# Optimization experiments

Hardware: AMD Instinct MI355X
Metric: run time of the kernel (lower is better)

## Reference

```python
import jax, jax.numpy as jnp
import numpy as np

N = 30000   # fluid particles
E = 480000  # edges
F = 4       # fluidFeatures (in channels)
P = 8       # RBF basis size per dim (dims=[8], 1D)
LAYERS = [32, 64, 64, 2]


def hat_basis(x, n):
    # 'linear' RBF: hat functions on n evenly spaced centers in [-1, 1]
    centers = jnp.linspace(-1.0, 1.0, n, dtype=x.dtype)
    spacing = 2.0 / (n - 1)
    return jnp.maximum(0.0, 1.0 - jnp.abs(x[:, None] - centers[None, :]) / spacing)  # [E, n]


def rbf_conv(x, fi, fj, d, W, b, mask, n_nodes):
    # x: [N, Cin]; d: [E, 1] clamped; W: [P, Cin, Cout]; b: [Cout]
    phi = hat_basis(d[:, 0], W.shape[0])      # [E, P]
    xj = x[fj]                                 # gather source features [E, Cin]
    msg = jnp.zeros((xj.shape[0], W.shape[2]), dtype=x.dtype)
    for p in range(W.shape[0]):                # small fixed P=8 loop keeps memory O(E*Cout)
        msg = msg + phi[:, p, None] * (xj @ W[p])
    msg = jnp.where(mask[:, None], msg, 0.0)   # centerIgnore: drop self edges fi==fj
    out = jax.ops.segment_sum(msg, fi, num_segments=n_nodes)  # scatter-reduce to targets
    return out + b


def _xavier(key, shape_in, shape_out):
    lim = float(np.sqrt(6.0 / (shape_in + shape_out)))
    return jax.random.uniform(key, (shape_in, shape_out), jnp.float32, -lim, lim)


def setup_inputs() -> dict:
    key = jax.random.key(0)
    ks = jax.random.split(key, 16)
    fluidFeatures = jax.random.normal(ks[0], (N, F), jnp.float32)
    fi = jax.random.randint(ks[1], (E,), 0, N)
    fj = jax.random.randint(ks[2], (E,), 0, N)
    distances = jax.random.normal(ks[3], (E, 1), jnp.float32)
    # conv channels: 4->32, 64->64, 64->64, 64->2
    cio = [(F, 32), (2 * 32, 64), (64, 64), (64, 2)]
    inp = {"fluidFeatures": fluidFeatures, "fi": fi, "fj": fj, "distances": distances}
    for li, (ci, co) in enumerate(cio):
        inp[f"cW{li}"] = jax.random.normal(ks[4 + li], (P, ci, co), jnp.float32) * (1.0 / np.sqrt(P * ci))
        inp[f"cb{li}"] = jnp.zeros((co,), jnp.float32)
        inp[f"fW{li}"] = _xavier(ks[8 + li], ci, co)   # stored [in, out]
        inp[f"fb{li}"] = jnp.zeros((co,), jnp.float32)
    return inp


def reference(fluidFeatures, fi, fj, distances,
              cW0, cb0, fW0, fb0, cW1, cb1, fW1, fb1,
              cW2, cb2, fW2, fb2, cW3, cb3, fW3, fb3):
    n_nodes = fluidFeatures.shape[0]
    mask = fi != fj                     # centerIgnore (mask instead of filter: jit-safe)
    d = jnp.clip(distances, -1.0, 1.0)

    conv0 = rbf_conv(fluidFeatures, fi, fj, d, cW0, cb0, mask, n_nodes)  # [N, 32]
    lin0 = fluidFeatures @ fW0 + fb0                                      # [N, 32]
    ans = jnp.concatenate([lin0, conv0], axis=1)                          # [N, 64]

    # i = 1: features[0]=32 != features[1]=64 -> no residual
    ansc = jax.nn.relu(ans)
    ans = rbf_conv(ansc, fi, fj, d, cW1, cb1, mask, n_nodes) + (ansc @ fW1 + fb1)
    # i = 2: features[1]==features[2]==64 and shapes match -> residual
    ansc = jax.nn.relu(ans)
    ans = rbf_conv(ansc, fi, fj, d, cW2, cb2, mask, n_nodes) + (ansc @ fW2 + fb2) + ans
    # i = 3: 64 -> 2, no residual
    ansc = jax.nn.relu(ans)
    ans = rbf_conv(ansc, fi, fj, d, cW3, cb3, mask, n_nodes) + (ansc @ fW3 + fb3)

    return ans  # dim == 1 (dims=[8]) -> no /128
```

## Files before the change

kernel.cpp:

```cpp
#include <hip/hip_runtime.h>


#define CAP 48

typedef __attribute__((ext_vector_type(8))) short short8;
typedef __attribute__((ext_vector_type(4))) float f32x4;
typedef int v4i __attribute__((ext_vector_type(4)));

__device__ __forceinline__ short bf16s(float f) {
  unsigned u = __float_as_uint(f);
  return (short)((u + 0x7FFF + ((u >> 16) & 1)) >> 16);
}
__device__ __forceinline__ float b2f(unsigned short s) {
  return __uint_as_float(((unsigned)s) << 16);
}
__device__ __forceinline__ unsigned pack2(float a, float b) {
  return (unsigned)(unsigned short)bf16s(a) | ((unsigned)(unsigned short)bf16s(b) << 16);
}
__device__ __forceinline__ float dec_w0(int v) {
  return __uint_as_float(0x3F800000u | (((unsigned)v & 0xFFFu) << 11)) - 1.0f;
}
__device__ __forceinline__ float dec_sf(int v) {
  return (float)(((unsigned)v >> 12) & 1u);
}
__device__ __forceinline__ unsigned long long rfl64(unsigned long long x) {
  unsigned lo = __builtin_amdgcn_readfirstlane((unsigned)x);
  unsigned hi = __builtin_amdgcn_readfirstlane((unsigned)(x >> 32));
  return ((unsigned long long)hi << 32) | (unsigned long long)lo;
}

#define LOAD_RECS32Q(JROW, CPTR, MRAW)                                      \
  v4i q0, q1, q2, q3, q4, q5, q6, q7;                                       \
  int MRAW;                                                                 \
  asm volatile("s_load_dwordx4 %0, %9, 0x0\n\t"                             \
               "s_load_dwordx4 %1, %9, 0x10\n\t"                            \
               "s_load_dwordx4 %2, %9, 0x20\n\t"                            \
               "s_load_dwordx4 %3, %9, 0x30\n\t"                            \
               "s_load_dwordx4 %4, %9, 0x40\n\t"                            \
               "s_load_dwordx4 %5, %9, 0x50\n\t"                            \
               "s_load_dwordx4 %6, %9, 0x60\n\t"                            \
               "s_load_dwordx4 %7, %9, 0x70\n\t"                            \
               "s_load_dword %8, %10, 0x0\n\t"                              \
               "s_waitcnt lgkmcnt(0)"                                       \
               : "=&s"(q0), "=&s"(q1), "=&s"(q2), "=&s"(q3), "=&s"(q4),     \
                 "=&s"(q5), "=&s"(q6), "=&s"(q7), "=&s"(MRAW)               \
               : "s"(JROW), "s"(CPTR)                                       \
               : "memory")

#define LOAD_RECS16TQ(JROW)                                                 \
  v4i qt0, qt1, qt2, qt3;                                                   \
  asm volatile("s_load_dwordx4 %0, %4, 0x80\n\t"                            \
               "s_load_dwordx4 %1, %4, 0x90\n\t"                            \
               "s_load_dwordx4 %2, %4, 0xA0\n\t"                            \
               "s_load_dwordx4 %3, %4, 0xB0\n\t"                            \
               "s_waitcnt lgkmcnt(0)"                                       \
               : "=&s"(qt0), "=&s"(qt1), "=&s"(qt2), "=&s"(qt3)             \
               : "s"(JROW)                                                  \
               : "memory")

#define RECK(K) ((K) < 4 ? q0[(K) & 3] : (K) < 8 ? q1[(K) & 3] :            \
                 (K) < 12 ? q2[(K) & 3] : (K) < 16 ? q3[(K) & 3] :          \
                 (K) < 20 ? q4[(K) & 3] : (K) < 24 ? q5[(K) & 3] :          \
                 (K) < 28 ? q6[(K) & 3] : q7[(K) & 3])
#define RECT(K) ((K) < 4 ? qt0[(K) & 3] : (K) < 8 ? qt1[(K) & 3] :          \
                 (K) < 12 ? qt2[(K) & 3] : qt3[(K) & 3])

__global__ void fill_prep(const float* __restrict__ dist,
                          const int* __restrict__ fi, const int* __restrict__ fj,
                          int* __restrict__ cnt, int* __restrict__ jw, int nE,
                          const float* __restrict__ cW0, const float* __restrict__ fW0,
                          const float* __restrict__ cW1, const float* __restrict__ fW1,
                          const float* __restrict__ cW2, const float* __restrict__ fW2,
                          const float* __restrict__ cW3,
                          short* __restrict__ W0T, short* __restrict__ W1T,
                          short* __restrict__ W2T, short* __restrict__ WT3,
                          const float* __restrict__ X,
                          unsigned short* __restrict__ Xb, int n,
                          int fillBlocks, int prepBlocks) {
  if ((int)blockIdx.x < fillBlocks) {
    int e = blockIdx.x * blockDim.x + threadIdx.x;
    if (e >= nE) return;
    int i = fi[e], j = fj[e];
    if (i == j) return;
    float d = fminf(1.0f, fmaxf(-1.0f, dist[e]));
    float u = (d + 1.0f) * 3.5f;
    int p = min((int)u, 6);
    float w0 = 1.0f - (u - (float)p);
    int wq = min((int)(w0 * 4096.0f + 0.5f), 4095);
    int pos = atomicAdd(&cnt[i], 1);
    if (pos < CAP)
      jw[(size_t)i * CAP + pos] =
          (int)(((unsigned)j << 17) | ((unsigned)p << 14) | 0x1000u | (unsigned)wq);
  } else if ((int)blockIdx.x < fillBlocks + prepBlocks) {
    int idx = ((int)blockIdx.x - fillBlocks) * blockDim.x + threadIdx.x;
    if (idx < 36864) {
      int o = idx / 576, k = idx - o * 576;
      float v = (k < 512) ? cW1[((size_t)(k >> 6) * 64 + (k & 63)) * 64 + o]
                          : fW1[(size_t)(k - 512) * 64 + o];
      W1T[idx] = bf16s(v);
    } else if (idx < 73728) {
      int r = idx - 36864;
      int o = r / 576, k = r - o * 576;
      float v = (k < 512) ? cW2[((size_t)(k >> 6) * 64 + (k & 63)) * 64 + o]
                          : fW2[(size_t)(k - 512) * 64 + o];
      W2T[r] = bf16s(v);
    } else if (idx < 77824) {
      int r = idx - 73728;
      int o = r >> 6, k = r & 63;
      float v = 0.0f;
      if (o < 32) {
        if (k >= 60) v = fW0[(size_t)(k - 60) * 32 + o];
      } else {
        if ((k & 7) < 4 && k < 60)
          v = cW0[((size_t)(k >> 3) * 4 + (k & 7)) * 32 + (o - 32)];
      }
      W0T[r] = bf16s(v);
    } else if (idx < 78848) {
      int r = idx - 77824;
      int t = r >> 6, ch = r & 63;
      WT3[r] = bf16s(cW3[((size_t)(t >> 1) * 64 + ch) * 2 + (t & 1)]);
    }
  } else {
    int idx = ((int)blockIdx.x - fillBlocks - prepBlocks) * blockDim.x + threadIdx.x;
    if (idx >= n * 8) return;
    int i = idx >> 3, c = idx & 7;
    float v = (c < 4) ? X[(size_t)i * 4 + c] : 0.0f;
    Xb[idx] = (unsigned short)bf16s(v);
  }
}

__global__ __launch_bounds__(1024, 8) void layer0_gemm(
    const unsigned short* __restrict__ Xb,
    const int* __restrict__ cnt, const int* __restrict__ jw,
    const float* __restrict__ cb0, const float* __restrict__ fb0,
    const short* __restrict__ W0T,
    unsigned short* __restrict__ ansc0, int n) {
  __shared__ __align__(16) unsigned short sA0[16 * 72];
  const int tid = threadIdx.x;
  const int w = tid >> 6;
  const int lane = tid & 63;
  const int s_lane = lane >> 3;
  const int k_lane = lane & 7;
  const int nodeBase = blockIdx.x * 16;
  const int i = nodeBase + w;
  const bool valid = (i < n);
  const int ic = valid ? i : 0;
  const int* jrow = (const int*)rfl64((unsigned long long)(jw + (size_t)ic * CAP));
  const int* cptr = (const int*)rfl64((unsigned long long)(cnt + ic));
  LOAD_RECS32Q(jrow, cptr, mraw);
  const int m = valid ? min(mraw, CAP) : 0;
  float acc = 0.0f;
#define L0E(K, RE)                                                          \
  { int v_ = RE(K);                                                         \
    const unsigned short* rp_ = Xb + ((size_t)((unsigned)v_ >> 17) << 3);   \
    float xv_ = b2f(rp_[k_lane]);                                           \
    float w0_ = dec_w0(v_);                                                 \
    float w1_ = dec_sf(v_) - w0_;                                           \
    int p_ = (int)(((unsigned)v_ >> 14) & 7u);                              \
    float sel_ = (s_lane == p_) ? w0_ : ((s_lane == p_ + 1) ? w1_ : 0.0f);  \
    acc = fmaf(sel_, xv_, acc); }
  L0E(0, RECK) L0E(1, RECK) L0E(2, RECK) L0E(3, RECK)
  L0E(4, RECK) L0E(5, RECK) L0E(6, RECK) L0E(7, RECK)
  L0E(8, RECK) L0E(9, RECK) L0E(10, RECK) L0E(11, RECK)
  L0E(12, RECK) L0E(13, RECK) L0E(14, RECK) L0E(15, RECK)
  if (m > 16) {
    L0E(16, RECK) L0E(17, RECK) L0E(18, RECK) L0E(19, RECK)
    L0E(20, RECK) L0E(21, RECK) L0E(22, RECK) L0E(23, RECK)
    L0E(24, RECK) L0E(25, RECK) L0E(26, RECK) L0E(27, RECK)
    L0E(28, RECK) L0E(29, RECK) L0E(30, RECK) L0E(31, RECK)
    if (m > 32) {
      LOAD_RECS16TQ(jrow);
      L0E(0, RECT) L0E(1, RECT) L0E(2, RECT) L0E(3, RECT)
      L0E(4, RECT) L0E(5, RECT) L0E(6, RECT) L0E(7, RECT)
      L0E(8, RECT) L0E(9, RECT) L0E(10, RECT) L0E(11, RECT)
      L0E(12, RECT) L0E(13, RECT) L0E(14, RECT) L0E(15, RECT)
    }
  }
#undef L0E
  float aout = acc;
  if (lane >= 60) aout = b2f(Xb[(size_t)ic * 8 + (lane - 60)]);
  sA0[w * 72 + lane] = (unsigned short)bf16s(aout);
  __syncthreads();
  if (w < 4) {
    const int mrow = lane & 15, quad = lane >> 4, t = w;
    short8 b0 = *(const short8*)(sA0 + mrow * 72 + quad * 8);
    short8 b1 = *(const short8*)(sA0 + mrow * 72 + quad * 8 + 32);
    short8 a0 = *(const short8*)(W0T + (size_t)(t * 16 + mrow) * 64 + quad * 8);
    short8 a1 = *(const short8*)(W0T + (size_t)(t * 16 + mrow) * 64 + quad * 8 + 32);
    f32x4 acc4 = {0, 0, 0, 0};
    acc4 = __builtin_amdgcn_mfma_f32_16x16x32_bf16(a0, b0, acc4, 0, 0, 0);
    acc4 = __builtin_amdgcn_mfma_f32_16x16x32_bf16(a1, b1, acc4, 0, 0, 0);
    const int node2 = nodeBase + mrow;
    const int ch0 = t * 16 + quad * 4;
    if (node2 < n) {
      float vv[4];
      #pragma unroll
      for (int r = 0; r < 4; ++r) {
        int ch = ch0 + r;
        float bias = (ch < 32) ? fb0[ch] : cb0[ch - 32];
        vv[r] = fmaxf(acc4[r] + bias, 0.0f);
      }
      *(uint2*)(ansc0 + (size_t)node2 * 64 + ch0) =
          make_uint2(pack2(vv[0], vv[1]), pack2(vv[2], vv[3]));
    }
  }
}

__global__ __launch_bounds__(1024, 8) void conv_agg(
    const unsigned short* __restrict__ ancPrev,
    const int* __restrict__ cnt, const int* __restrict__ jw,
    const short* __restrict__ WTn,
    const float* __restrict__ cb, const float* __restrict__ fb,
    const float* __restrict__ resid,
    float* __restrict__ outF32,
    unsigned short* __restrict__ outAnsc,
    const short* __restrict__ WT3,
    float* __restrict__ T, int flags, int n) {
  __shared__ __align__(16) unsigned short sA[16 * 584];
  __shared__ __align__(16) unsigned short sC[16 * 72];
  const int tid = threadIdx.x;
  const int w = tid >> 6;
  const int lane = tid & 63;
  const int nodeBase = blockIdx.x * 16;
  const int i = nodeBase + w;
  const bool valid = (i < n);
  const int ic = valid ? i : 0;
  const int* jrow = (const int*)rfl64((unsigned long long)(jw + (size_t)ic * CAP));
  const int* cptr = (const int*)rfl64((unsigned long long)(cnt + ic));
  LOAD_RECS32Q(jrow, cptr, mraw);
  const int m = valid ? min(mraw, CAP) : 0;
  const unsigned short own = ancPrev[(size_t)ic * 64 + lane];
  float a0 = 0, a1 = 0, a2 = 0, a3 = 0, a4 = 0, a5 = 0, a6 = 0, a7 = 0;
#define CVE(K, RE)                                                          \
  { int v_ = RE(K);                                                         \
    const unsigned short* rp_ = ancPrev + ((size_t)((unsigned)v_ >> 17) << 6); \
    float xv_ = b2f(rp_[lane]);                                             \
    float w0_ = dec_w0(v_);                                                 \
    float w1_ = dec_sf(v_) - w0_;                                           \
    switch (((unsigned)v_ >> 14) & 7u) {                                    \
      case 0: a0 = fmaf(w0_, xv_, a0); a1 = fmaf(w1_, xv_, a1); break;      \
      case 1: a1 = fmaf(w0_, xv_, a1); a2 = fmaf(w1_, xv_, a2); break;      \
      case 2: a2 = fmaf(w0_, xv_, a2); a3 = fmaf(w1_, xv_, a3); break;      \
      case 3: a3 = fmaf(w0_, xv_, a3); a4 = fmaf(w1_, xv_, a4); break;      \
      case 4: a4 = fmaf(w0_, xv_, a4); a5 = fmaf(w1_, xv_, a5); break;      \
      case 5: a5 = fmaf(w0_, xv_, a5); a6 = fmaf(w1_, xv_, a6); break;      \
      case 6: a6 = fmaf(w0_, xv_, a6); a7 = fmaf(w1_, xv_, a7); break;      \
      default: break;                                                       \
    } }
  CVE(0, RECK) CVE(1, RECK) CVE(2, RECK) CVE(3, RECK)
  CVE(4, RECK) CVE(5, RECK) CVE(6, RECK) CVE(7, RECK)
  CVE(8, RECK) CVE(9, RECK) CVE(10, RECK) CVE(11, RECK)
  CVE(12, RECK) CVE(13, RECK) CVE(14, RECK) CVE(15, RECK)
  if (m > 16) {
    CVE(16, RECK) CVE(17, RECK) CVE(18, RECK) CVE(19, RECK)
    CVE(20, RECK) CVE(21, RECK) CVE(22, RECK) CVE(23, RECK)
    CVE(24, RECK) CVE(25, RECK) CVE(26, RECK) CVE(27, RECK)
    CVE(28, RECK) CVE(29, RECK) CVE(30, RECK) CVE(31, RECK)
    if (m > 32) {
      LOAD_RECS16TQ(jrow);
      CVE(0, RECT) CVE(1, RECT) CVE(2, RECT) CVE(3, RECT)
      CVE(4, RECT) CVE(5, RECT) CVE(6, RECT) CVE(7, RECT)
      CVE(8, RECT) CVE(9, RECT) CVE(10, RECT) CVE(11, RECT)
      CVE(12, RECT) CVE(13, RECT) CVE(14, RECT) CVE(15, RECT)
    }
  }
#undef CVE
  {
    unsigned short* sAr = sA + w * 584;
    sAr[0 * 64 + lane] = (unsigned short)bf16s(a0);
    sAr[1 * 64 + lane] = (unsigned short)bf16s(a1);
    sAr[2 * 64 + lane] = (unsigned short)bf16s(a2);
    sAr[3 * 64 + lane] = (unsigned short)bf16s(a3);
    sAr[4 * 64 + lane] = (unsigned short)bf16s(a4);
    sAr[5 * 64 + lane] = (unsigned short)bf16s(a5);
    sAr[6 * 64 + lane] = (unsigned short)bf16s(a6);
    sAr[7 * 64 + lane] = (unsigned short)bf16s(a7);
    sAr[512 + lane] = own;
  }
  __syncthreads();
  if (w < 4) {
    const int mrow = lane & 15, quad = lane >> 4, t = w;
    f32x4 acc4 = {0, 0, 0, 0};
    const short* arow = WTn + (size_t)(t * 16 + mrow) * 576 + quad * 8;
    const unsigned short* brow = sA + mrow * 584 + quad * 8;
    #pragma unroll
    for (int kk = 0; kk < 18; ++kk) {
      short8 af = *(const short8*)(arow + kk * 32);
      short8 bf = *(const short8*)(brow + kk * 32);
      acc4 = __builtin_amdgcn_mfma_f32_16x16x32_bf16(af, bf, acc4, 0, 0, 0);
    }
    const int node2 = nodeBase + mrow;
    const int ch0 = t * 16 + quad * 4;
    if (node2 < n) {
      float4 rv = make_float4(0.f, 0.f, 0.f, 0.f);
      if (flags & 1) rv = *(const float4*)(resid + (size_t)node2 * 64 + ch0);
      float v0 = acc4[0] + cb[ch0 + 0] + fb[ch0 + 0] + rv.x;
      float v1 = acc4[1] + cb[ch0 + 1] + fb[ch0 + 1] + rv.y;
      float v2 = acc4[2] + cb[ch0 + 2] + fb[ch0 + 2] + rv.z;
      float v3 = acc4[3] + cb[ch0 + 3] + fb[ch0 + 3] + rv.w;
      if (flags & 2) {
        *(float2*)(outF32 + (size_t)node2 * 64 + ch0) = make_float2(v0, v1);
        *(float2*)(outF32 + (size_t)node2 * 64 + ch0 + 2) = make_float2(v2, v3);
      }
      unsigned lo = pack2(fmaxf(v0, 0.f), fmaxf(v1, 0.f));
      unsigned hi = pack2(fmaxf(v2, 0.f), fmaxf(v3, 0.f));
      *(uint2*)(outAnsc + (size_t)node2 * 64 + ch0) = make_uint2(lo, hi);
      if (flags & 4) {
        *(unsigned*)(sC + mrow * 72 + ch0) = lo;
        *(unsigned*)(sC + mrow * 72 + ch0 + 2) = hi;
      }
    } else if (flags & 4) {
      *(unsigned*)(sC + mrow * 72 + ch0) = 0u;
      *(unsigned*)(sC + mrow * 72 + ch0 + 2) = 0u;
    }
  }
  if (flags & 4) {
    __syncthreads();
    if (w == 0) {
      const int mrow = lane & 15, quad = lane >> 4;
      short8 b0 = *(const short8*)(sC + mrow * 72 + quad * 8);
      short8 b1 = *(const short8*)(sC + mrow * 72 + quad * 8 + 32);
      short8 a0v = *(const short8*)(WT3 + mrow * 64 + quad * 8);
      short8 a1v = *(const short8*)(WT3 + mrow * 64 + quad * 8 + 32);
      f32x4 acc4 = {0, 0, 0, 0};
      acc4 = __builtin_amdgcn_mfma_f32_16x16x32_bf16(a0v, b0, acc4, 0, 0, 0);
      acc4 = __builtin_amdgcn_mfma_f32_16x16x32_bf16(a1v, b1, acc4, 0, 0, 0);
      const int node2 = nodeBase + mrow;
      if (node2 < n) {
        float* tr = T + (size_t)node2 * 18 + quad * 4;
        *(float2*)(tr) = make_float2(acc4[0], acc4[1]);
        *(float2*)(tr + 2) = make_float2(acc4[2], acc4[3]);
      }
    }
  }
}

__global__ __launch_bounds__(256, 4) void layer3_kernel(
    const unsigned short* __restrict__ Xb,
    const float* __restrict__ T,
    const int* __restrict__ cnt, const int* __restrict__ jw,
    const float* __restrict__ cb3, const float* __restrict__ fb3,
    const float* __restrict__ fW3,
    float* __restrict__ out, int n) {
  const int lane = threadIdx.x & 63;
  const int i = (blockIdx.x * blockDim.x + threadIdx.x) >> 6;
  if (i >= n) return;
  const int m = min(cnt[i], CAP);
  float c0 = 0.0f, c1 = 0.0f;
  if (lane < m) {
    int v = jw[(size_t)i * CAP + lane];
    unsigned j = (unsigned)v >> 17;
    unsigned p = ((unsigned)v >> 14) & 7u;
    unsigned off9 = j * 9u + p;
    float w0 = dec_w0(v);
    float w1 = 1.0f - w0;
    const float* tb = T + (size_t)off9 * 2;
    float2 ta = *(const float2*)(tb);
    float2 tc = *(const float2*)(tb + 2);
    c0 = w0 * ta.x + w1 * tc.x;
    c1 = w0 * ta.y + w1 * tc.y;
  }
  float xi = b2f(Xb[(size_t)i * 64 + lane]);
  float2 fw = *(const float2*)(fW3 + lane * 2);
  c0 = fmaf(xi, fw.x, c0);
  c1 = fmaf(xi, fw.y, c1);
  #pragma unroll
  for (int off = 32; off > 0; off >>= 1) {
    c0 += __shfl_xor(c0, off, 64);
    c1 += __shfl_xor(c1, off, 64);
  }
  if (lane == 0) {
    out[(size_t)i * 2 + 0] = c0 + cb3[0] + fb3[0];
    out[(size_t)i * 2 + 1] = c1 + cb3[1] + fb3[1];
  }
}

extern "C" void kernel_launch(void* const* d_in, const int* in_sizes, int n_in,
                              void* d_out, int out_size, void* d_ws, size_t ws_size,
                              hipStream_t stream) {
  const float* X    = (const float*)d_in[0];
  const int*   fi   = (const int*)d_in[1];
  const int*   fj   = (const int*)d_in[2];
  const float* dist = (const float*)d_in[3];
  const float* cW0 = (const float*)d_in[4];  const float* cb0 = (const float*)d_in[5];
  const float* fW0 = (const float*)d_in[6];  const float* fb0 = (const float*)d_in[7];
  const float* cW1 = (const float*)d_in[8];  const float* cb1 = (const float*)d_in[9];
  const float* fW1 = (const float*)d_in[10]; const float* fb1 = (const float*)d_in[11];
  const float* cW2 = (const float*)d_in[12]; const float* cb2 = (const float*)d_in[13];
  const float* fW2 = (const float*)d_in[14]; const float* fb2 = (const float*)d_in[15];
  const float* cW3 = (const float*)d_in[16]; const float* cb3 = (const float*)d_in[17];
  const float* fW3 = (const float*)d_in[18]; const float* fb3 = (const float*)d_in[19];
  float* out = (float*)d_out;

  const int n  = in_sizes[0] / 4;
  const int nE = in_sizes[1];

  unsigned short* ansc0 = (unsigned short*)d_ws;
  float*          ans1  = (float*)(ansc0 + (size_t)n * 64);
  unsigned short* ansc1 = (unsigned short*)(ans1 + (size_t)n * 64);
  unsigned short* ansc2 = ansc1 + (size_t)n * 64;
  float*          T     = (float*)(ansc2 + (size_t)n * 64);
  unsigned short* Xb16  = (unsigned short*)(T + (size_t)n * 18);
  short* W1T = (short*)(Xb16 + (size_t)n * 8);
  short* W2T = W1T + 36864;
  short* W0T = W2T + 36864;
  short* WT3 = W0T + 4096;
  int*   jw  = (int*)(WT3 + 1024);
  int*   cnt = jw + (size_t)n * CAP;

  hipMemsetAsync(jw, 0, ((size_t)n * CAP + n) * sizeof(int), stream);
  const int fillBlocks = (nE + 255) / 256;
  const int prepBlocks = (78848 + 255) / 256;
  const int xbBlocks   = (n * 8 + 255) / 256;
  fill_prep<<<fillBlocks + prepBlocks + xbBlocks, 256, 0, stream>>>(
      dist, fi, fj, cnt, jw, nE, cW0, fW0, cW1, fW1, cW2, fW2, cW3,
      W0T, W1T, W2T, WT3, X, Xb16, n, fillBlocks, prepBlocks);

  const int nodeBlocks = (n + 15) / 16;
  layer0_gemm<<<nodeBlocks, 1024, 0, stream>>>(Xb16, cnt, jw, cb0, fb0,
                                               W0T, ansc0, n);
  conv_agg<<<nodeBlocks, 1024, 0, stream>>>(ansc0, cnt, jw, W1T, cb1, fb1,
                                            ans1 , ans1, ansc1,
                                            WT3, T, 2, n);
  conv_agg<<<nodeBlocks, 1024, 0, stream>>>(ansc1, cnt, jw, W2T, cb2, fb2,
                                            ans1, ans1, ansc2,
                                            WT3, T, 5, n);
  layer3_kernel<<<(n * 64 + 255) / 256, 256, 0, stream>>>(ansc2, T, cnt, jw,
                                                          cb3, fb3, fW3, out, n);
}
```

Measured before the change: 268.9 us.

## Restructure edge aggregation into batched dword gathers and unify layer0 into conv_agg

The per-edge gather in conv_agg now has each wave half handle a different edge and fetch two bf16 channels per lane with one dword load. Batches of eight such loads are issued through inline asm before one wait, and the two halves are combined with a cross-half shuffle. Weight fragments for the MFMA stage are loaded in batched asm dwordx4 groups, and biases are pre-summed into a BIA buffer. Layer 0 drops its dedicated kernel and reuses conv_agg by padding the input to 64 channels and expanding W0T to the 576-wide layout, which adds redundant MFMA work and a larger padded input.

After: 258.9 us. -3.7%, faster.

```diff
diff --git a/kernel.cpp b/kernel.cpp
--- a/kernel.cpp
+++ b/kernel.cpp
@@ -69,11 +69,15 @@
                           const int* __restrict__ fi, const int* __restrict__ fj,
                           int* __restrict__ cnt, int* __restrict__ jw, int nE,
                           const float* __restrict__ cW0, const float* __restrict__ fW0,
+                          const float* __restrict__ cb0, const float* __restrict__ fb0,
                           const float* __restrict__ cW1, const float* __restrict__ fW1,
+                          const float* __restrict__ cb1, const float* __restrict__ fb1,
                           const float* __restrict__ cW2, const float* __restrict__ fW2,
+                          const float* __restrict__ cb2, const float* __restrict__ fb2,
                           const float* __restrict__ cW3,
                           short* __restrict__ W0T, short* __restrict__ W1T,
                           short* __restrict__ W2T, short* __restrict__ WT3,
+                          float* __restrict__ BIA,
                           const float* __restrict__ X,
                           unsigned short* __restrict__ Xb, int n,
                           int fillBlocks, int prepBlocks) {
@@ -104,113 +108,45 @@
       float v = (k < 512) ? cW2[((size_t)(k >> 6) * 64 + (k & 63)) * 64 + o]
                           : fW2[(size_t)(k - 512) * 64 + o];
       W2T[r] = bf16s(v);
-    } else if (idx < 77824) {
+    } else if (idx < 110592) {
       int r = idx - 73728;
-      int o = r >> 6, k = r & 63;
+      int o = r / 576, k = r - o * 576;
       float v = 0.0f;
-      if (o < 32) {
-        if (k >= 60) v = fW0[(size_t)(k - 60) * 32 + o];
+      if (k < 512) {
+        int s = k >> 6, ci = k & 63;
+        if (ci < 4 && o >= 32) v = cW0[((size_t)s * 4 + ci) * 32 + (o - 32)];
       } else {
-        if ((k & 7) < 4 && k < 60)
-          v = cW0[((size_t)(k >> 3) * 4 + (k & 7)) * 32 + (o - 32)];
+        int c = k - 512;
+        if (c < 4 && o < 32) v = fW0[(size_t)c * 32 + o];
       }
       W0T[r] = bf16s(v);
-    } else if (idx < 78848) {
-      int r = idx - 77824;
+    } else if (idx < 111616) {
+      int r = idx - 110592;
       int t = r >> 6, ch = r & 63;
       WT3[r] = bf16s(cW3[((size_t)(t >> 1) * 64 + ch) * 2 + (t & 1)]);
+    } else if (idx < 111808) {
+      int r = idx - 111616;
+      int layer = r >> 6, ch = r & 63;
+      float v;
+      if (layer == 0) v = (ch < 32) ? fb0[ch] : cb0[ch - 32];
+      else if (layer == 1) v = cb1[ch] + fb1[ch];
+      else v = cb2[ch] + fb2[ch];
+      BIA[r] = v;
     }
   } else {
     int idx = ((int)blockIdx.x - fillBlocks - prepBlocks) * blockDim.x + threadIdx.x;
-    if (idx >= n * 8) return;
-    int i = idx >> 3, c = idx & 7;
+    if (idx >= n * 64) return;
+    int i = idx >> 6, c = idx & 63;
     float v = (c < 4) ? X[(size_t)i * 4 + c] : 0.0f;
     Xb[idx] = (unsigned short)bf16s(v);
   }
 }
 
-__global__ __launch_bounds__(1024, 8) void layer0_gemm(
-    const unsigned short* __restrict__ Xb,
-    const int* __restrict__ cnt, const int* __restrict__ jw,
-    const float* __restrict__ cb0, const float* __restrict__ fb0,
-    const short* __restrict__ W0T,
-    unsigned short* __restrict__ ansc0, int n) {
-  __shared__ __align__(16) unsigned short sA0[16 * 72];
-  const int tid = threadIdx.x;
-  const int w = tid >> 6;
-  const int lane = tid & 63;
-  const int s_lane = lane >> 3;
-  const int k_lane = lane & 7;
-  const int nodeBase = blockIdx.x * 16;
-  const int i = nodeBase + w;
-  const bool valid = (i < n);
-  const int ic = valid ? i : 0;
-  const int* jrow = (const int*)rfl64((unsigned long long)(jw + (size_t)ic * CAP));
-  const int* cptr = (const int*)rfl64((unsigned long long)(cnt + ic));
-  LOAD_RECS32Q(jrow, cptr, mraw);
-  const int m = valid ? min(mraw, CAP) : 0;
-  float acc = 0.0f;
-#define L0E(K, RE)                                                          \
-  { int v_ = RE(K);                                                         \
-    const unsigned short* rp_ = Xb + ((size_t)((unsigned)v_ >> 17) << 3);   \
-    float xv_ = b2f(rp_[k_lane]);                                           \
-    float w0_ = dec_w0(v_);                                                 \
-    float w1_ = dec_sf(v_) - w0_;                                           \
-    int p_ = (int)(((unsigned)v_ >> 14) & 7u);                              \
-    float sel_ = (s_lane == p_) ? w0_ : ((s_lane == p_ + 1) ? w1_ : 0.0f);  \
-    acc = fmaf(sel_, xv_, acc); }
-  L0E(0, RECK) L0E(1, RECK) L0E(2, RECK) L0E(3, RECK)
-  L0E(4, RECK) L0E(5, RECK) L0E(6, RECK) L0E(7, RECK)
-  L0E(8, RECK) L0E(9, RECK) L0E(10, RECK) L0E(11, RECK)
-  L0E(12, RECK) L0E(13, RECK) L0E(14, RECK) L0E(15, RECK)
-  if (m > 16) {
-    L0E(16, RECK) L0E(17, RECK) L0E(18, RECK) L0E(19, RECK)
-    L0E(20, RECK) L0E(21, RECK) L0E(22, RECK) L0E(23, RECK)
-    L0E(24, RECK) L0E(25, RECK) L0E(26, RECK) L0E(27, RECK)
-    L0E(28, RECK) L0E(29, RECK) L0E(30, RECK) L0E(31, RECK)
-    if (m > 32) {
-      LOAD_RECS16TQ(jrow);
-      L0E(0, RECT) L0E(1, RECT) L0E(2, RECT) L0E(3, RECT)
-      L0E(4, RECT) L0E(5, RECT) L0E(6, RECT) L0E(7, RECT)
-      L0E(8, RECT) L0E(9, RECT) L0E(10, RECT) L0E(11, RECT)
-      L0E(12, RECT) L0E(13, RECT) L0E(14, RECT) L0E(15, RECT)
-    }
-  }
-#undef L0E
-  float aout = acc;
-  if (lane >= 60) aout = b2f(Xb[(size_t)ic * 8 + (lane - 60)]);
-  sA0[w * 72 + lane] = (unsigned short)bf16s(aout);
-  __syncthreads();
-  if (w < 4) {
-    const int mrow = lane & 15, quad = lane >> 4, t = w;
-    short8 b0 = *(const short8*)(sA0 + mrow * 72 + quad * 8);
-    short8 b1 = *(const short8*)(sA0 + mrow * 72 + quad * 8 + 32);
-    short8 a0 = *(const short8*)(W0T + (size_t)(t * 16 + mrow) * 64 + quad * 8);
-    short8 a1 = *(const short8*)(W0T + (size_t)(t * 16 + mrow) * 64 + quad * 8 + 32);
-    f32x4 acc4 = {0, 0, 0, 0};
-    acc4 = __builtin_amdgcn_mfma_f32_16x16x32_bf16(a0, b0, acc4, 0, 0, 0);
-    acc4 = __builtin_amdgcn_mfma_f32_16x16x32_bf16(a1, b1, acc4, 0, 0, 0);
-    const int node2 = nodeBase + mrow;
-    const int ch0 = t * 16 + quad * 4;
-    if (node2 < n) {
-      float vv[4];
-      #pragma unroll
-      for (int r = 0; r < 4; ++r) {
-        int ch = ch0 + r;
-        float bias = (ch < 32) ? fb0[ch] : cb0[ch - 32];
-        vv[r] = fmaxf(acc4[r] + bias, 0.0f);
-      }
-      *(uint2*)(ansc0 + (size_t)node2 * 64 + ch0) =
-          make_uint2(pack2(vv[0], vv[1]), pack2(vv[2], vv[3]));
-    }
-  }
-}
-
 __global__ __launch_bounds__(1024, 8) void conv_agg(
-    const unsigned short* __restrict__ ancPrev,
+    const unsigned short* __restrict__ prev,
     const int* __restrict__ cnt, const int* __restrict__ jw,
     const short* __restrict__ WTn,
-    const float* __restrict__ cb, const float* __restrict__ fb,
+    const float* __restrict__ bias,
     const float* __restrict__ resid,
     float* __restrict__ outF32,
     unsigned short* __restrict__ outAnsc,
@@ -221,6 +157,9 @@
   const int tid = threadIdx.x;
   const int w = tid >> 6;
   const int lane = tid & 63;
+  const int half = lane >> 5;
+  const int l32 = lane & 31;
+  const unsigned ln4 = (unsigned)l32 * 4u;
   const int nodeBase = blockIdx.x * 16;
   const int i = nodeBase + w;
   const bool valid = (i < n);
@@ -229,81 +168,134 @@
   const int* cptr = (const int*)rfl64((unsigned long long)(cnt + ic));
   LOAD_RECS32Q(jrow, cptr, mraw);
   const int m = valid ? min(mraw, CAP) : 0;
-  const unsigned short own = ancPrev[(size_t)ic * 64 + lane];
-  float a0 = 0, a1 = 0, a2 = 0, a3 = 0, a4 = 0, a5 = 0, a6 = 0, a7 = 0;
-#define CVE(K, RE)                                                          \
-  { int v_ = RE(K);                                                         \
-    const unsigned short* rp_ = ancPrev + ((size_t)((unsigned)v_ >> 17) << 6); \
-    float xv_ = b2f(rp_[lane]);                                             \
-    float w0_ = dec_w0(v_);                                                 \
-    float w1_ = dec_sf(v_) - w0_;                                           \
-    switch (((unsigned)v_ >> 14) & 7u) {                                    \
-      case 0: a0 = fmaf(w0_, xv_, a0); a1 = fmaf(w1_, xv_, a1); break;      \
-      case 1: a1 = fmaf(w0_, xv_, a1); a2 = fmaf(w1_, xv_, a2); break;      \
-      case 2: a2 = fmaf(w0_, xv_, a2); a3 = fmaf(w1_, xv_, a3); break;      \
-      case 3: a3 = fmaf(w0_, xv_, a3); a4 = fmaf(w1_, xv_, a4); break;      \
-      case 4: a4 = fmaf(w0_, xv_, a4); a5 = fmaf(w1_, xv_, a5); break;      \
-      case 5: a5 = fmaf(w0_, xv_, a5); a6 = fmaf(w1_, xv_, a6); break;      \
-      case 6: a6 = fmaf(w0_, xv_, a6); a7 = fmaf(w1_, xv_, a7); break;      \
-      default: break;                                                       \
-    } }
-  CVE(0, RECK) CVE(1, RECK) CVE(2, RECK) CVE(3, RECK)
-  CVE(4, RECK) CVE(5, RECK) CVE(6, RECK) CVE(7, RECK)
-  CVE(8, RECK) CVE(9, RECK) CVE(10, RECK) CVE(11, RECK)
-  CVE(12, RECK) CVE(13, RECK) CVE(14, RECK) CVE(15, RECK)
+  const unsigned short own = prev[(size_t)ic * 64 + lane];
+  float aL0 = 0, aL1 = 0, aL2 = 0, aL3 = 0, aL4 = 0, aL5 = 0, aL6 = 0, aL7 = 0;
+  float aH0 = 0, aH1 = 0, aH2 = 0, aH3 = 0, aH4 = 0, aH5 = 0, aH6 = 0, aH7 = 0;
+  unsigned u0, u1, u2, u3, u4, u5, u6, u7;
+  int v0, v1, v2, v3, v4, v5, v6, v7;
+#define GSET(G, EA, EB)                                                     \
+  { v##G = half ? (EB) : (EA);                                              \
+    u##G = ((((unsigned)v##G) >> 10) & 0xFFFFFF80u) + ln4; }
+#define GISSUE8(BASE)                                                       \
+  asm volatile("global_load_dword %0, %0, %[bb]\n\t"                        \
+               "global_load_dword %1, %1, %[bb]\n\t"                        \
+               "global_load_dword %2, %2, %[bb]\n\t"                        \
+               "global_load_dword %3, %3, %[bb]\n\t"                        \
+               "global_load_dword %4, %4, %[bb]\n\t"                        \
+               "global_load_dword %5, %5, %[bb]\n\t"                        \
+               "global_load_dword %6, %6, %[bb]\n\t"                        \
+               "global_load_dword %7, %7, %[bb]\n\t"                        \
+               "s_waitcnt vmcnt(0)"                                         \
+               : "+v"(u0), "+v"(u1), "+v"(u2), "+v"(u3),                    \
+                 "+v"(u4), "+v"(u5), "+v"(u6), "+v"(u7)                     \
+               : [bb] "s"(BASE)                                             \
+               : "memory")
+#define SLOT1(S)                                                            \
+  { float sel_ = (p_ == (S)) ? w0_ : (p_ == ((S)-1)) ? w1_ : 0.0f;          \
+    aL##S = fmaf(sel_, xl_, aL##S);                                         \
+    aH##S = fmaf(sel_, xh_, aH##S); }
+#define GCONS(G)                                                            \
+  { int vv_ = v##G;                                                         \
+    unsigned uu_ = u##G;                                                    \
+    float w0_ = dec_w0(vv_);                                                \
+    float w1_ = dec_sf(vv_) - w0_;                                          \
+    int p_ = (int)(((unsigned)vv_ >> 14) & 7u);                             \
+    float xl_ = __uint_as_float(uu_ << 16);                                 \
+    float xh_ = __uint_as_float(uu_ & 0xFFFF0000u);                         \
+    SLOT1(0) SLOT1(1) SLOT1(2) SLOT1(3) SLOT1(4) SLOT1(5) SLOT1(6) SLOT1(7) }
+  GSET(0, RECK(0), RECK(1))   GSET(1, RECK(2), RECK(3))
+  GSET(2, RECK(4), RECK(5))   GSET(3, RECK(6), RECK(7))
+  GSET(4, RECK(8), RECK(9))   GSET(5, RECK(10), RECK(11))
+  GSET(6, RECK(12), RECK(13)) GSET(7, RECK(14), RECK(15))
+  GISSUE8(prev);
+  GCONS(0) GCONS(1) GCONS(2) GCONS(3) GCONS(4) GCONS(5) GCONS(6) GCONS(7)
   if (m > 16) {
-    CVE(16, RECK) CVE(17, RECK) CVE(18, RECK) CVE(19, RECK)
-    CVE(20, RECK) CVE(21, RECK) CVE(22, RECK) CVE(23, RECK)
-    CVE(24, RECK) CVE(25, RECK) CVE(26, RECK) CVE(27, RECK)
-    CVE(28, RECK) CVE(29, RECK) CVE(30, RECK) CVE(31, RECK)
+    GSET(0, RECK(16), RECK(17)) GSET(1, RECK(18), RECK(19))
+    GSET(2, RECK(20), RECK(21)) GSET(3, RECK(22), RECK(23))
+    GSET(4, RECK(24), RECK(25)) GSET(5, RECK(26), RECK(27))
+    GSET(6, RECK(28), RECK(29)) GSET(7, RECK(30), RECK(31))
+    GISSUE8(prev);
+    GCONS(0) GCONS(1) GCONS(2) GCONS(3) GCONS(4) GCONS(5) GCONS(6) GCONS(7)
     if (m > 32) {
       LOAD_RECS16TQ(jrow);
-      CVE(0, RECT) CVE(1, RECT) CVE(2, RECT) CVE(3, RECT)
-      CVE(4, RECT) CVE(5, RECT) CVE(6, RECT) CVE(7, RECT)
-      CVE(8, RECT) CVE(9, RECT) CVE(10, RECT) CVE(11, RECT)
-      CVE(12, RECT) CVE(13, RECT) CVE(14, RECT) CVE(15, RECT)
+      GSET(0, RECT(0), RECT(1))   GSET(1, RECT(2), RECT(3))
+      GSET(2, RECT(4), RECT(5))   GSET(3, RECT(6), RECT(7))
+      GSET(4, RECT(8), RECT(9))   GSET(5, RECT(10), RECT(11))
+      GSET(6, RECT(12), RECT(13)) GSET(7, RECT(14), RECT(15))
+      GISSUE8(prev);
+      GCONS(0) GCONS(1) GCONS(2) GCONS(3) GCONS(4) GCONS(5) GCONS(6) GCONS(7)
     }
   }
-#undef CVE
-  {
-    unsigned short* sAr = sA + w * 584;
-    sAr[0 * 64 + lane] = (unsigned short)bf16s(a0);
-    sAr[1 * 64 + lane] = (unsigned short)bf16s(a1);
-    sAr[2 * 64 + lane] = (unsigned short)bf16s(a2);
-    sAr[3 * 64 + lane] = (unsigned short)bf16s(a3);
-    sAr[4 * 64 + lane] = (unsigned short)bf16s(a4);
-    sAr[5 * 64 + lane] = (unsigned short)bf16s(a5);
-    sAr[6 * 64 + lane] = (unsigned short)bf16s(a6);
-    sAr[7 * 64 + lane] = (unsigned short)bf16s(a7);
-    sAr[512 + lane] = own;
-  }
+#undef GSET
+#undef GISSUE8
+#undef SLOT1
+#undef GCONS
+#define RED(S)                                                              \
+  aL##S += __shfl_xor(aL##S, 32, 64);                                       \
+  aH##S += __shfl_xor(aH##S, 32, 64);
+  RED(0) RED(1) RED(2) RED(3) RED(4) RED(5) RED(6) RED(7)
+#undef RED
+  unsigned short* sAr = sA + w * 584;
+  if (half == 0) {
+#define SWR(S) ((unsigned*)(sAr + (S)*64))[l32] = pack2(aL##S, aH##S);
+    SWR(0) SWR(1) SWR(2) SWR(3) SWR(4) SWR(5) SWR(6) SWR(7)
+#undef SWR
+  }
+  sAr[512 + lane] = own;
   __syncthreads();
+
   if (w < 4) {
     const int mrow = lane & 15, quad = lane >> 4, t = w;
+    const unsigned rowoff = (unsigned)((t * 16 + mrow) * 1152 + quad * 16);
+    const unsigned short* brow = sA + mrow * 584 + quad * 8;
     f32x4 acc4 = {0, 0, 0, 0};
-    const short* arow = WTn + (size_t)(t * 16 + mrow) * 576 + quad * 8;
-    const unsigned short* brow = sA + mrow * 584 + quad * 8;
-    #pragma unroll
-    for (int kk = 0; kk < 18; ++kk) {
-      short8 af = *(const short8*)(arow + kk * 32);
-      short8 bf = *(const short8*)(brow + kk * 32);
-      acc4 = __builtin_amdgcn_mfma_f32_16x16x32_bf16(af, bf, acc4, 0, 0, 0);
-    }
+    short8 f0, f1, f2, f3, f4, f5;
+#define WLOAD6(CO)                                                          \
+  asm volatile("global_load_dwordx4 %0, %[vo], %[bb] offset:0\n\t"          \
+               "global_load_dwordx4 %1, %[vo], %[bb] offset:64\n\t"         \
+               "global_load_dwordx4 %2, %[vo], %[bb] offset:128\n\t"        \
+               "global_load_dwordx4 %3, %[vo], %[bb] offset:192\n\t"        \
+               "global_load_dwordx4 %4, %[vo], %[bb] offset:256\n\t"        \
+               "global_load_dwordx4 %5, %[vo], %[bb] offset:320\n\t"        \
+               "s_waitcnt vmcnt(0)"                                         \
+               : "=&v"(f0), "=&v"(f1), "=&v"(f2), "=&v"(f3),                \
+                 "=&v"(f4), "=&v"(f5)                                       \
+               : [vo] "v"(rowoff + (CO)), [bb] "s"(WTn)                     \
+               : "memory")
+#define MM6(KK0)                                                            \
+  acc4 = __builtin_amdgcn_mfma_f32_16x16x32_bf16(                           \
+      f0, *(const short8*)(brow + ((KK0) + 0) * 32), acc4, 0, 0, 0);        \
+  acc4 = __builtin_amdgcn_mfma_f32_16x16x32_bf16(                           \
+      f1, *(const short8*)(brow + ((KK0) + 1) * 32), acc4, 0, 0, 0);        \
+  acc4 = __builtin_amdgcn_mfma_f32_16x16x32_bf16(                           \
+      f2, *(const short8*)(brow + ((KK0) + 2) * 32), acc4, 0, 0, 0);        \
+  acc4 = __builtin_amdgcn_mfma_f32_16x16x32_bf16(                           \
+      f3, *(const short8*)(brow + ((KK0) + 3) * 32), acc4, 0, 0, 0);        \
+  acc4 = __builtin_amdgcn_mfma_f32_16x16x32_bf16(                           \
+      f4, *(const short8*)(brow + ((KK0) + 4) * 32), acc4, 0, 0, 0);        \
+  acc4 = __builtin_amdgcn_mfma_f32_16x16x32_bf16(                           \
+      f5, *(const short8*)(brow + ((KK0) + 5) * 32), acc4, 0, 0, 0);
+    WLOAD6(0);    MM6(0);
+    WLOAD6(384);  MM6(6);
+    WLOAD6(768);  MM6(12);
+#undef WLOAD6
+#undef MM6
     const int node2 = nodeBase + mrow;
     const int ch0 = t * 16 + quad * 4;
     if (node2 < n) {
+      float4 bb4 = *(const float4*)(bias + ch0);
       float4 rv = make_float4(0.f, 0.f, 0.f, 0.f);
       if (flags & 1) rv = *(const float4*)(resid + (size_t)node2 * 64 + ch0);
-      float v0 = acc4[0] + cb[ch0 + 0] + fb[ch0 + 0] + rv.x;
-      float v1 = acc4[1] + cb[ch0 + 1] + fb[ch0 + 1] + rv.y;
-      float v2 = acc4[2] + cb[ch0 + 2] + fb[ch0 + 2] + rv.z;
-      float v3 = acc4[3] + cb[ch0 + 3] + fb[ch0 + 3] + rv.w;
+      float o0 = acc4[0] + bb4.x + rv.x;
+      float o1 = acc4[1] + bb4.y + rv.y;
+      float o2 = acc4[2] + bb4.z + rv.z;
+      float o3 = acc4[3] + bb4.w + rv.w;
       if (flags & 2) {
-        *(float2*)(outF32 + (size_t)node2 * 64 + ch0) = make_float2(v0, v1);
-        *(float2*)(outF32 + (size_t)node2 * 64 + ch0 + 2) = make_float2(v2, v3);
+        *(float2*)(outF32 + (size_t)node2 * 64 + ch0) = make_float2(o0, o1);
+        *(float2*)(outF32 + (size_t)node2 * 64 + ch0 + 2) = make_float2(o2, o3);
       }
-      unsigned lo = pack2(fmaxf(v0, 0.f), fmaxf(v1, 0.f));
-      unsigned hi = pack2(fmaxf(v2, 0.f), fmaxf(v3, 0.f));
+      unsigned lo = pack2(fmaxf(o0, 0.f), fmaxf(o1, 0.f));
+      unsigned hi = pack2(fmaxf(o2, 0.f), fmaxf(o3, 0.f));
       *(uint2*)(outAnsc + (size_t)node2 * 64 + ch0) = make_uint2(lo, hi);
       if (flags & 4) {
         *(unsigned*)(sC + mrow * 72 + ch0) = lo;
@@ -401,30 +393,30 @@
   unsigned short* ansc2 = ansc1 + (size_t)n * 64;
   float*          T     = (float*)(ansc2 + (size_t)n * 64);
   unsigned short* Xb16  = (unsigned short*)(T + (size_t)n * 18);
-  short* W1T = (short*)(Xb16 + (size_t)n * 8);
+  short* W1T = (short*)(Xb16 + (size_t)n * 64);
   short* W2T = W1T + 36864;
   short* W0T = W2T + 36864;
-  short* WT3 = W0T + 4096;
-  int*   jw  = (int*)(WT3 + 1024);
+  short* WT3 = W0T + 36864;
+  float* BIA = (float*)(WT3 + 1024);
+  int*   jw  = (int*)(BIA + 192);
   int*   cnt = jw + (size_t)n * CAP;
 
   hipMemsetAsync(jw, 0, ((size_t)n * CAP + n) * sizeof(int), stream);
   const int fillBlocks = (nE + 255) / 256;
-  const int prepBlocks = (78848 + 255) / 256;
-  const int xbBlocks   = (n * 8 + 255) / 256;
+  const int prepBlocks = (111808 + 255) / 256;
+  const int xbBlocks   = (n * 64 + 255) / 256;
   fill_prep<<<fillBlocks + prepBlocks + xbBlocks, 256, 0, stream>>>(
-      dist, fi, fj, cnt, jw, nE, cW0, fW0, cW1, fW1, cW2, fW2, cW3,
-      W0T, W1T, W2T, WT3, X, Xb16, n, fillBlocks, prepBlocks);
+      dist, fi, fj, cnt, jw, nE,
+      cW0, fW0, cb0, fb0, cW1, fW1, cb1, fb1, cW2, fW2, cb2, fb2, cW3,
+      W0T, W1T, W2T, WT3, BIA, X, Xb16, n, fillBlocks, prepBlocks);
 
   const int nodeBlocks = (n + 15) / 16;
-  layer0_gemm<<<nodeBlocks, 1024, 0, stream>>>(Xb16, cnt, jw, cb0, fb0,
-                                               W0T, ansc0, n);
-  conv_agg<<<nodeBlocks, 1024, 0, stream>>>(ansc0, cnt, jw, W1T, cb1, fb1,
-                                            ans1 , ans1, ansc1,
-                                            WT3, T, 2, n);
-  conv_agg<<<nodeBlocks, 1024, 0, stream>>>(ansc1, cnt, jw, W2T, cb2, fb2,
-                                            ans1, ans1, ansc2,
-                                            WT3, T, 5, n);
+  conv_agg<<<nodeBlocks, 1024, 0, stream>>>(Xb16, cnt, jw, W0T, BIA,
+                                            ans1, ans1, ansc0, WT3, T, 0, n);
+  conv_agg<<<nodeBlocks, 1024, 0, stream>>>(ansc0, cnt, jw, W1T, BIA + 64,
+                                            ans1, ans1, ansc1, WT3, T, 2, n);
+  conv_agg<<<nodeBlocks, 1024, 0, stream>>>(ansc1, cnt, jw, W2T, BIA + 128,
+                                            ans1, ans1, ansc2, WT3, T, 5, n);
   layer3_kernel<<<(n * 64 + 255) / 256, 256, 0, stream>>>(ansc2, T, cnt, jw,
                                                           cb3, fb3, fW3, out, n);
 }
```
